# Optimization experiments

Hardware: AMD Instinct MI355X
Metric: run time of the kernel (lower is better)

The kernel has to match this reference:

```python
import jax, jax.numpy as jnp
import numpy as np
from math import gcd, pi

Q = 16  # max_period
W = 16  # window (FIR taps), causal

def _ramanujan_sum_vec(q, W):
    n = np.arange(W, dtype=np.float64)
    ks = [a for a in range(1, q + 1) if gcd(a, q) == 1]
    if len(ks) == 0:
        return np.ones(W, dtype=np.float64)
    angles = np.outer(np.asarray(ks, dtype=np.float64), n) * (2.0 * pi / q)
    c = np.cos(angles).sum(axis=0)
    c = c - c.mean()
    denom = np.sqrt(max((c * c).sum(), 1e-6))
    return c / denom

# [Q, 1, W] Ramanujan FIR bank (buffer, non-trainable)
RAMA_K = jnp.asarray(np.stack([_ramanujan_sum_vec(q, W) for q in range(1, Q + 1)])[:, None, :].astype(np.float32))

def _fir_bank(x):
    """x: [N, 1, T] causal-padded by W-1 on the left already? No: pad here. Returns [N, Q, T]."""
    xp = jnp.pad(x, ((0, 0), (0, 0), (W - 1, 0)))  # causal left pad
    return jax.lax.conv_general_dilated(
        xp, RAMA_K.astype(x.dtype), window_strides=(1,), padding='VALID',
        dimension_numbers=('NCH', 'OIH', 'NCH'))

def setup_inputs() -> dict:
    key = jax.random.key(0)
    k = jax.random.split(key, 4)
    B, T, M, D = 8, 512, 8, 128
    return {
        'z': jax.random.normal(k[0], (B, T, M, D), dtype=jnp.float32),
        'valid_mask': jnp.ones((B, T, M), dtype=jnp.float32),
        'gate_w1': jax.random.normal(k[1], (Q,), dtype=jnp.float32),
        'gate_b1': jnp.zeros((Q,), dtype=jnp.float32),
        'gate_w2': jax.random.normal(k[2], (Q, Q), dtype=jnp.float32) * (1.0 / np.sqrt(Q)),
        'gate_b2': jnp.zeros((Q,), dtype=jnp.float32),
        'beta': jnp.full((1,), 0.5, dtype=jnp.float32),
    }

def reference(z, valid_mask, gate_w1, gate_b1, gate_w2, gate_b2, beta):
    B, T, M, D = z.shape
    # analysis signal: mean over D (proj_dim=0), masked
    z_anl = z.mean(axis=-1) * valid_mask                      # [B,T,M]
    x = z_anl.transpose(0, 2, 1).reshape(B * M, 1, T)         # [B*M,1,T]
    r = _fir_bank(x)                                          # [B*M,Q,T]
    r = r.reshape(B, M, Q, T).transpose(0, 2, 1, 3)           # [B,Q,M,T]
    # faithful replication of torch's r.view(B*M, Q, T) on the [B,Q,M,T] contiguous tensor
    rg = r.reshape(B * M, Q, T)
    h1 = jax.nn.gelu(rg * gate_w1[None, :, None] + gate_b1[None, :, None], approximate=False)
    g = jax.nn.sigmoid(jnp.einsum('nqt,pq->npt', h1, gate_w2) + gate_b2[None, :, None])  # [B*M,Q,T]
    g = g.reshape(B, M, Q, T).transpose(0, 2, 1, 3)           # [B,Q,M,T]
    # synthesis branch: FIR bank applied per (b,m,d) channel
    z_syn = (z * valid_mask[..., None]).transpose(0, 2, 3, 1)  # [B,M,D,T]
    y = z_syn.reshape(B * M * D, 1, T)
    R = _fir_bank(y)                                          # [B*M*D,Q,T]
    R = R.reshape(B, M, D, Q, T).transpose(0, 3, 1, 2, 4)     # [B,Q,M,D,T]
    p = jnp.einsum('bqmdt,bqmt->bmdt', R, g)                  # gated sum over Q -> [B,M,D,T]
    p = p.transpose(0, 3, 1, 2)                               # [B,T,M,D]
    h = z + beta[0] * p
    vm = valid_mask[..., None]
    h = vm * h + (1.0 - vm) * z
    return h
```

## Files before the change

### kernel.cpp

```cpp
#include <hip/hip_runtime.h>
#include <math.h>

#define NB 8
#define NT 512
#define NM 8
#define ND 128
#define TC 16

__device__ __constant__ short RAMA_C[256] = {
    1,1,1,1,1,1,1,1,1,1,1,1,1,1,1,1,
    1,-1,1,-1,1,-1,1,-1,1,-1,1,-1,1,-1,1,-1,
    2,-1,-1,2,-1,-1,2,-1,-1,2,-1,-1,2,-1,-1,2,
    2,0,-2,0,2,0,-2,0,2,0,-2,0,2,0,-2,0,
    4,-1,-1,-1,-1,4,-1,-1,-1,-1,4,-1,-1,-1,-1,4,
    2,1,-1,-2,-1,1,2,1,-1,-2,-1,1,2,1,-1,-2,
    6,-1,-1,-1,-1,-1,-1,6,-1,-1,-1,-1,-1,-1,6,-1,
    4,0,0,0,-4,0,0,0,4,0,0,0,-4,0,0,0,
    6,0,0,-3,0,0,-3,0,0,6,0,0,-3,0,0,-3,
    4,1,-1,1,-1,-4,-1,1,-1,1,4,1,-1,1,-1,-4,
    10,-1,-1,-1,-1,-1,-1,-1,-1,-1,-1,10,-1,-1,-1,-1,
    4,0,2,0,-2,0,-4,0,-2,0,2,0,4,0,2,0,
    12,-1,-1,-1,-1,-1,-1,-1,-1,-1,-1,-1,-1,12,-1,-1,
    6,1,-1,1,-1,1,-1,-6,-1,1,-1,1,-1,1,6,1,
    8,1,1,-2,1,-4,-2,1,1,-2,-4,1,-2,1,1,8,
    8,0,0,0,0,0,0,0,-8,0,0,0,0,0,0,0
};

__global__ __launch_bounds__(512, 1) void rama_one_k(
    const float* __restrict__ z, const float* __restrict__ vm,
    const float* __restrict__ gw1, const float* __restrict__ gb1,
    const float* __restrict__ gw2, const float* __restrict__ gb2,
    const float* __restrict__ beta,
    float* __restrict__ out)
{
    __shared__ float Ks[256];
    __shared__ float za_s[31][9];
    __shared__ float vm_s[31][9];
    __shared__ __align__(16) float effs[8][16][16];

    const int tid  = threadIdx.x;
    const int wv   = tid >> 6;
    const int lane = tid & 63;
    const int blk  = blockIdx.x;
    const int tc   = blk & 31;
    const int b    = blk >> 5;
    const int t0   = tc * TC;
    const int m    = wv;

    if (tid < 256) {
        const int q = tid >> 4;
        float sum = 0.0f, ss = 0.0f;
        #pragma unroll
        for (int j = 0; j < 16; ++j) sum += (float)RAMA_C[q * 16 + j];
        const float mean = sum * (1.0f / 16.0f);
        #pragma unroll
        for (int j = 0; j < 16; ++j) {
            const float d = (float)RAMA_C[q * 16 + j] - mean;
            ss += d * d;
        }
        Ks[tid] = ((float)RAMA_C[tid] - mean) / sqrtf(fmaxf(ss, 1e-6f));
    }

    if (lane < 31) {
        const int tt = t0 - 15 + lane;
        vm_s[lane][m] = (tt >= 0) ? vm[((size_t)b * NT + tt) * NM + m] : 0.0f;
    }
    float2 zr[31];
    #pragma unroll
    for (int j = 0; j < 31; ++j) {
        const int tt = t0 - 15 + j;
        if (tt >= 0) {
            zr[j] = *(const float2*)(z + (((size_t)b * NT + tt) * NM + m) * ND + lane * 2);
        } else { zr[j].x = 0.0f; zr[j].y = 0.0f; }
    }
    #pragma unroll
    for (int j = 0; j < 31; ++j) {
        float s = zr[j].x + zr[j].y;
        #pragma unroll
        for (int off = 32; off; off >>= 1) s += __shfl_xor(s, off, 64);
        if (lane == 0) za_s[j][m] = s * (1.0f / 128.0f) * vm_s[j][m];
    }
    __syncthreads();

    if (tid < 128) {
        const int gm = tid >> 4;
        const int gi = tid & 15;
        float rg[16];
        #pragma unroll
        for (int q = 0; q < 16; ++q) rg[q] = 0.0f;
        #pragma unroll
        for (int dly = 0; dly < 16; ++dly) {
            const int j  = gi + 15 - dly;
            const float k0 = Ks[(2 * gm)     * 16 + 15 - dly];
            const float k1 = Ks[(2 * gm + 1) * 16 + 15 - dly];
            #pragma unroll
            for (int m2 = 0; m2 < 8; ++m2) {
                const float zv = za_s[j][m2];
                rg[m2]     = fmaf(k0, zv, rg[m2]);
                rg[8 + m2] = fmaf(k1, zv, rg[8 + m2]);
            }
        }
        float h1[16];
        #pragma unroll
        for (int q = 0; q < 16; ++q) {
            const float v = fmaf(rg[q], gw1[q], gb1[q]);
            h1[q] = 0.5f * v * (1.0f + erff(v * 0.70710678118654752440f));
        }
        float g[16];
        #pragma unroll
        for (int p = 0; p < 16; ++p) {
            float acc = gb2[p];
            #pragma unroll
            for (int q = 0; q < 16; ++q) acc = fmaf(h1[q], gw2[p * 16 + q], acc);
            g[p] = 1.0f / (1.0f + expf(-acc));
        }
        const float sc = beta[0] * vm_s[gi + 15][gm];
        float eff16[16];
        #pragma unroll
        for (int dly = 0; dly < 16; ++dly) {
            float acc = 0.0f;
            #pragma unroll
            for (int p = 0; p < 16; ++p) acc = fmaf(Ks[p * 16 + 15 - dly], g[p], acc);
            eff16[dly] = acc * vm_s[gi + 15 - dly][gm] * sc;
        }
        float4* ep = (float4*)&effs[gm][gi][0];
        ep[0] = make_float4(eff16[0],  eff16[1],  eff16[2],  eff16[3]);
        ep[1] = make_float4(eff16[4],  eff16[5],  eff16[6],  eff16[7]);
        ep[2] = make_float4(eff16[8],  eff16[9],  eff16[10], eff16[11]);
        ep[3] = make_float4(eff16[12], eff16[13], eff16[14], eff16[15]);
    }
    __syncthreads();

    #pragma unroll
    for (int i = 0; i < TC; ++i) {
        const float4 e0 = *(const float4*)&effs[m][i][0];
        const float4 e1 = *(const float4*)&effs[m][i][4];
        const float4 e2 = *(const float4*)&effs[m][i][8];
        const float4 e3 = *(const float4*)&effs[m][i][12];
        float px = 0.0f, py = 0.0f;
        #define ACC(EV, DLY) { const float2 zv = zr[15 + i - (DLY)]; \
                               px = fmaf((EV), zv.x, px); py = fmaf((EV), zv.y, py); }
        ACC(e0.x, 0)  ACC(e0.y, 1)  ACC(e0.z, 2)  ACC(e0.w, 3)
        ACC(e1.x, 4)  ACC(e1.y, 5)  ACC(e1.z, 6)  ACC(e1.w, 7)
        ACC(e2.x, 8)  ACC(e2.y, 9)  ACC(e2.z, 10) ACC(e2.w, 11)
        ACC(e3.x, 12) ACC(e3.y, 13) ACC(e3.z, 14) ACC(e3.w, 15)
        #undef ACC
        const float2 zraw = zr[15 + i];
        float2 hv;
        hv.x = zraw.x + px;
        hv.y = zraw.y + py;
        const int t = t0 + i;
        *(float2*)(out + (((size_t)b * NT + t) * NM + m) * ND + lane * 2) = hv;
    }
}

extern "C" void kernel_launch(void* const* d_in, const int* in_sizes, int n_in,
                              void* d_out, int out_size, void* d_ws, size_t ws_size,
                              hipStream_t stream) {
    const float* z    = (const float*)d_in[0];
    const float* vm   = (const float*)d_in[1];
    const float* gw1  = (const float*)d_in[2];
    const float* gb1  = (const float*)d_in[3];
    const float* gw2  = (const float*)d_in[4];
    const float* gb2  = (const float*)d_in[5];
    const float* beta = (const float*)d_in[6];
    float* out = (float*)d_out;

    rama_one_k<<<NB * (NT / TC), 512, 0, stream>>>(
        z, vm, gw1, gb1, gw2, gb2, beta, out);
}
```

Before: 28.38 us.

## Halve time tile, spread gate compute across all waves, drop block barrier

The time tile per block shrinks from 16 to 8 steps, which doubles the grid to 512 blocks, and launch bounds now request up to 4 blocks per CU. The gate MLP, previously run by only the first 128 threads (two waves), now runs in every wave, each handling its own m over 8 lanes. Because each wave writes and reads only its own effs[m] slice, the second __syncthreads becomes a wave barrier. The cost is a larger halo: each block loads 23 rows of z for 8 outputs instead of 31 for 16, so redundant z reads go up.

```diff
diff --git a/kernel.cpp b/kernel.cpp
--- a/kernel.cpp
+++ b/kernel.cpp
@@ -5,7 +5,8 @@
 #define NT 512
 #define NM 8
 #define ND 128
-#define TC 16
+#define TC 8
+#define WIN (TC + 15)
 
 __device__ __constant__ short RAMA_C[256] = {
     1,1,1,1,1,1,1,1,1,1,1,1,1,1,1,1,
@@ -26,7 +27,7 @@
     8,0,0,0,0,0,0,0,-8,0,0,0,0,0,0,0
 };
 
-__global__ __launch_bounds__(512, 1) void rama_one_k(
+__global__ __launch_bounds__(512, 4) void rama_one_k(
     const float* __restrict__ z, const float* __restrict__ vm,
     const float* __restrict__ gw1, const float* __restrict__ gb1,
     const float* __restrict__ gw2, const float* __restrict__ gb2,
@@ -34,16 +35,16 @@
     float* __restrict__ out)
 {
     __shared__ float Ks[256];
-    __shared__ float za_s[31][9];
-    __shared__ float vm_s[31][9];
-    __shared__ __align__(16) float effs[8][16][16];
+    __shared__ float za_s[WIN][9];
+    __shared__ float vm_s[WIN][9];
+    __shared__ __align__(16) float effs[8][TC][16];
 
     const int tid  = threadIdx.x;
     const int wv   = tid >> 6;
     const int lane = tid & 63;
     const int blk  = blockIdx.x;
-    const int tc   = blk & 31;
-    const int b    = blk >> 5;
+    const int tc   = blk & 63;
+    const int b    = blk >> 6;
     const int t0   = tc * TC;
     const int m    = wv;
 
@@ -61,20 +62,20 @@
         Ks[tid] = ((float)RAMA_C[tid] - mean) / sqrtf(fmaxf(ss, 1e-6f));
     }
 
-    if (lane < 31) {
+    if (lane < WIN) {
         const int tt = t0 - 15 + lane;
         vm_s[lane][m] = (tt >= 0) ? vm[((size_t)b * NT + tt) * NM + m] : 0.0f;
     }
-    float2 zr[31];
+    float2 zr[WIN];
     #pragma unroll
-    for (int j = 0; j < 31; ++j) {
+    for (int j = 0; j < WIN; ++j) {
         const int tt = t0 - 15 + j;
         if (tt >= 0) {
             zr[j] = *(const float2*)(z + (((size_t)b * NT + tt) * NM + m) * ND + lane * 2);
         } else { zr[j].x = 0.0f; zr[j].y = 0.0f; }
     }
     #pragma unroll
-    for (int j = 0; j < 31; ++j) {
+    for (int j = 0; j < WIN; ++j) {
         float s = zr[j].x + zr[j].y;
         #pragma unroll
         for (int off = 32; off; off >>= 1) s += __shfl_xor(s, off, 64);
@@ -82,17 +83,16 @@
     }
     __syncthreads();
 
-    if (tid < 128) {
-        const int gm = tid >> 4;
-        const int gi = tid & 15;
+    if (lane < TC) {
+        const int gi = lane;
         float rg[16];
         #pragma unroll
         for (int q = 0; q < 16; ++q) rg[q] = 0.0f;
         #pragma unroll
         for (int dly = 0; dly < 16; ++dly) {
             const int j  = gi + 15 - dly;
-            const float k0 = Ks[(2 * gm)     * 16 + 15 - dly];
-            const float k1 = Ks[(2 * gm + 1) * 16 + 15 - dly];
+            const float k0 = Ks[(2 * m)     * 16 + 15 - dly];
+            const float k1 = Ks[(2 * m + 1) * 16 + 15 - dly];
             #pragma unroll
             for (int m2 = 0; m2 < 8; ++m2) {
                 const float zv = za_s[j][m2];
@@ -114,22 +114,22 @@
             for (int q = 0; q < 16; ++q) acc = fmaf(h1[q], gw2[p * 16 + q], acc);
             g[p] = 1.0f / (1.0f + expf(-acc));
         }
-        const float sc = beta[0] * vm_s[gi + 15][gm];
+        const float sc = beta[0] * vm_s[gi + 15][m];
         float eff16[16];
         #pragma unroll
         for (int dly = 0; dly < 16; ++dly) {
             float acc = 0.0f;
             #pragma unroll
             for (int p = 0; p < 16; ++p) acc = fmaf(Ks[p * 16 + 15 - dly], g[p], acc);
-            eff16[dly] = acc * vm_s[gi + 15 - dly][gm] * sc;
+            eff16[dly] = acc * vm_s[gi + 15 - dly][m] * sc;
         }
-        float4* ep = (float4*)&effs[gm][gi][0];
+        float4* ep = (float4*)&effs[m][gi][0];
         ep[0] = make_float4(eff16[0],  eff16[1],  eff16[2],  eff16[3]);
         ep[1] = make_float4(eff16[4],  eff16[5],  eff16[6],  eff16[7]);
         ep[2] = make_float4(eff16[8],  eff16[9],  eff16[10], eff16[11]);
         ep[3] = make_float4(eff16[12], eff16[13], eff16[14], eff16[15]);
     }
-    __syncthreads();
+    __builtin_amdgcn_wave_barrier();
 
     #pragma unroll
     for (int i = 0; i < TC; ++i) {
```

Result: slower. 82.42 us (+190.4%).
